# Kernel tuning notes

Hardware: AMD Instinct MI355X
Metric: run time of the kernel (lower is better)

Reference implementation:

```python
import jax, jax.numpy as jnp
import numpy as np

B, S, D = 2, 2048, 1024
H = 16
HD = D // H

def setup_inputs() -> dict:
    key = jax.random.key(0)
    ks = jax.random.split(key, 9)
    scale = 1.0 / np.sqrt(D)
    return {
        "qi": jax.random.normal(ks[0], (B, S, D), jnp.float32),
        "ki": jax.random.normal(ks[1], (B, S, D), jnp.float32),
        "vi": jax.random.normal(ks[2], (B, S, D), jnp.float32),
        "Wq": jax.random.normal(ks[3], (D, D), jnp.float32) * scale,
        "Wq_def": jax.random.normal(ks[4], (D, D), jnp.float32) * scale,
        "Wk": jax.random.normal(ks[5], (D, D), jnp.float32) * scale,
        "Wk_def": jax.random.normal(ks[6], (D, D), jnp.float32) * scale,
        "Wv": jax.random.normal(ks[7], (D, D), jnp.float32) * scale,
        "Wo": jax.random.normal(ks[8], (D, D), jnp.float32) * scale,
    }

def _heads(x, W):
    # torch Linear: x @ W.T, then view (B,S,H,HD) and transpose -> (B,H,S,HD)
    return (x @ W.T).reshape(B, S, H, HD).transpose(0, 2, 1, 3)

def reference(qi, ki, vi, Wq, Wq_def, Wk, Wk_def, Wv, Wo):
    q = _heads(qi, Wq)
    q_def = _heads(qi, Wq_def)
    k = _heads(ki, Wk)
    k_def = _heads(ki, Wk_def)
    v = _heads(vi, Wv)
    inv_sqrt = 1.0 / jnp.sqrt(jnp.asarray(HD, qi.dtype))
    scores = jnp.einsum('bhse,bhte->bhst', q, k) * inv_sqrt
    def_scores = jnp.einsum('bhse,bhte->bhst', q_def, k_def) * inv_sqrt
    # defeasible weights: sigmoid(def_scores).sum over t -> [B,H,S], broadcast over query dim
    def_w = jax.nn.sigmoid(def_scores).sum(axis=3)  # [B,H,S]
    attn = jax.nn.softmax(scores * def_w[:, :, None, :], axis=-1)
    attended = jnp.einsum('bhst,bhtd->bshd', attn, v).reshape(B, S, D)
    return attended @ Wo.T
```

## Files before the change

### kernel.cpp

```cpp
#include <hip/hip_runtime.h>
#include <math.h>

#define BSZ 2
#define SEQ 2048
#define DIM 1024
#define NH 16
#define HDIM 64
#define MR (BSZ*SEQ)

typedef __attribute__((ext_vector_type(8))) short bf16x8;
typedef __attribute__((ext_vector_type(4))) short bf16x4;
typedef __attribute__((ext_vector_type(4))) float floatx4;
typedef _Float16 f16x8 __attribute__((ext_vector_type(8)));

static __device__ __forceinline__ unsigned short f2bf(float x) {
    unsigned u = __float_as_uint(x);
    u += 0x7fffu + ((u >> 16) & 1u);
    return (unsigned short)(u >> 16);
}
static __device__ __forceinline__ float bf2f(unsigned short h) {
    return __uint_as_float(((unsigned)h) << 16);
}
static __device__ __forceinline__ unsigned short f2h(float x) {
    union { _Float16 h; unsigned short u; } v;
    v.h = (_Float16)x;
    return v.u;
}
static __device__ __forceinline__ float fexp2(float x) {
#if __has_builtin(__builtin_amdgcn_exp2f)
    return __builtin_amdgcn_exp2f(x);
#else
    return __expf(x * 0.69314718055994531f);
#endif
}
static __device__ __forceinline__ bf16x4 pack_bf16x4(float a, float b, float c, float d) {
    union { unsigned u[2]; bf16x4 v; } r;
    asm("v_cvt_pk_bf16_f32 %0, %1, %2" : "=v"(r.u[0]) : "v"(a), "v"(b));
    asm("v_cvt_pk_bf16_f32 %0, %1, %2" : "=v"(r.u[1]) : "v"(c), "v"(d));
    return r.v;
}
#define MFMA16(a,b,c) __builtin_amdgcn_mfma_f32_16x16x32_bf16((a),(b),(c),0,0,0)

static __device__ __forceinline__ floatx4 mfma_f16(bf16x8 a, bf16x8 b, floatx4 c) {
    union { bf16x8 s; f16x8 h; } ua, ub;
    ua.s = a; ub.s = b;
    return __builtin_amdgcn_mfma_f32_16x16x32_f16(ua.h, ub.h, c, 0, 0, 0);
}

static __device__ __forceinline__ floatx4 pv_mfma(bf16x4 a, bf16x4 b, floatx4 c) {
#if __has_builtin(__builtin_amdgcn_mfma_f32_16x16x16bf16_1k)
    return __builtin_amdgcn_mfma_f32_16x16x16bf16_1k(a, b, c, 0, 0, 0);
#else
    bf16x8 a8 = {a[0],a[1],a[2],a[3],0,0,0,0};
    bf16x8 b8 = {b[0],b[1],b[2],b[3],0,0,0,0};
    return MFMA16(a8, b8, c);
#endif
}

static __device__ __forceinline__ void gld16(const void* g, void* l) {
    __builtin_amdgcn_global_load_lds(
        (const __attribute__((address_space(1))) void*)g,
        (__attribute__((address_space(3))) void*)l, 16, 0, 0);
}

__global__ __launch_bounds__(256)
void conv_split(const float* p0, const float* p1, const float* p2,
                const float* p3,
                unsigned short* o0, unsigned short* o1, unsigned short* o2,
                unsigned short* o3,
                int r0, int r1, int r2, int r3)
{
    const float* pin; unsigned short* pout; int rows;
    switch (blockIdx.y) {
        case 0: pin=p0; pout=o0; rows=r0; break;
        case 1: pin=p1; pout=o1; rows=r1; break;
        case 2: pin=p2; pout=o2; rows=r2; break;
        default: pin=p3; pout=o3; rows=r3; break;
    }
    size_t idx = (size_t)blockIdx.x * 256 + threadIdx.x;
    if (idx * 4 >= (size_t)rows * DIM) return;
    size_t row = (idx * 4) >> 10;
    int col = (int)((idx * 4) & 1023);
    float4 f = *(const float4*)(pin + idx * 4);
    ushort4 h, l;
    h.x = f2bf(f.x); l.x = f2bf(f.x - bf2f(h.x));
    h.y = f2bf(f.y); l.y = f2bf(f.y - bf2f(h.y));
    h.z = f2bf(f.z); l.z = f2bf(f.z - bf2f(h.z));
    h.w = f2bf(f.w); l.w = f2bf(f.w - bf2f(h.w));
    *(ushort4*)(pout + row * 2048 + col)        = h;
    *(ushort4*)(pout + row * 2048 + 1024 + col) = l;
}

__global__ __launch_bounds__(256)
void conv_f16(const float* p0, const float* p1, const float* p2, const float* p3,
              unsigned short* o0, unsigned short* o1, unsigned short* o2,
              unsigned short* o3, int r0, int r1, int r2, int r3)
{
    const float* pin; unsigned short* pout; int rows;
    switch (blockIdx.y) {
        case 0: pin=p0; pout=o0; rows=r0; break;
        case 1: pin=p1; pout=o1; rows=r1; break;
        case 2: pin=p2; pout=o2; rows=r2; break;
        default: pin=p3; pout=o3; rows=r3; break;
    }
    size_t idx = (size_t)blockIdx.x * 256 + threadIdx.x;
    if (idx * 4 >= (size_t)rows * DIM) return;
    float4 f = *(const float4*)(pin + idx * 4);
    ushort4 h;
    h.x = f2h(f.x); h.y = f2h(f.y); h.z = f2h(f.z); h.w = f2h(f.w);
    *(ushort4*)(pout + idx * 4) = h;
}

__global__ __launch_bounds__(256)
void conv_hi(const float* p0, const float* p1, const float* p2,
             unsigned short* o0, unsigned short* o1, unsigned short* o2,
             int n0, int n1, int n2)
{
    const float* pin; unsigned short* pout; int n;
    switch (blockIdx.y) {
        case 0: pin=p0; pout=o0; n=n0; break;
        case 1: pin=p1; pout=o1; n=n1; break;
        default: pin=p2; pout=o2; n=n2; break;
    }
    size_t idx = (size_t)blockIdx.x * 256 + threadIdx.x;
    if (idx * 4 >= (size_t)n) return;
    float4 f = *(const float4*)(pin + idx * 4);
    ushort4 h;
    h.x = f2bf(f.x); h.y = f2bf(f.y); h.z = f2bf(f.z); h.w = f2bf(f.w);
    *(ushort4*)(pout + idx * 4) = h;
}

template<int EPI, bool SPLIT3, int DT>
__global__ __launch_bounds__(256)
void gemm_mfma(const unsigned short* __restrict__ A0, const unsigned short* __restrict__ A1,
               const unsigned short* __restrict__ B0, const unsigned short* __restrict__ B1,
               void* C0v, void* C1v, int lda, int ldb, int nkb)
{
    const unsigned short* A = blockIdx.z ? A1 : A0;
    const unsigned short* B = blockIdx.z ? B1 : B0;
    float* Cf = (float*)(blockIdx.z ? C1v : C0v);
    unsigned short* Cb = (unsigned short*)(blockIdx.z ? C1v : C0v);

    __shared__ __align__(16) unsigned short As[128][64];
    __shared__ __align__(16) unsigned short Bs[128][64];

    const int tid = threadIdx.x;
    const int lane = tid & 63, wv = tid >> 6;
    const int c = lane & 15, quad = lane >> 4;
    const int wm = wv >> 1, wn = wv & 1;
    const int rowBase = blockIdx.y << 7;
    const int colBase = blockIdx.x << 7;

    floatx4 acc[4][4];
#pragma unroll
    for (int i = 0; i < 4; ++i)
#pragma unroll
        for (int j = 0; j < 4; ++j) acc[i][j] = (floatx4){0.f,0.f,0.f,0.f};

    for (int kb = 0; kb < nkb; ++kb) {
        int aoff, boff;
        if (SPLIT3) {
            int t = kb >> 4, kk = (kb & 15) << 6;
            aoff = ((t == 1) ? 1024 : 0) + kk;
            boff = ((t == 2) ? 1024 : 0) + kk;
        } else { aoff = boff = kb << 6; }
        __syncthreads();
#pragma unroll
        for (int i = 0; i < 4; ++i) {
            int f = tid + (i << 8);
            int r = f >> 3, ch = (f & 7) << 3;
            gld16(A + (size_t)(rowBase + r) * lda + aoff + ch,
                  &As[0][0] + (size_t)f * 8);
            gld16(B + (size_t)(colBase + r) * ldb + boff + ch,
                  &Bs[0][0] + (size_t)f * 8);
        }
        __syncthreads();
#pragma unroll
        for (int ks = 0; ks < 2; ++ks) {
            bf16x8 af[4], bfr[4];
#pragma unroll
            for (int i = 0; i < 4; ++i) {
                af[i]  = *(const bf16x8*)&As[wm*64 + i*16 + c][ks*32 + quad*8];
                bfr[i] = *(const bf16x8*)&Bs[wn*64 + i*16 + c][ks*32 + quad*8];
            }
#pragma unroll
            for (int mi = 0; mi < 4; ++mi)
#pragma unroll
                for (int ni = 0; ni < 4; ++ni) {
                    if (DT == 0) acc[mi][ni] = MFMA16(af[mi], bfr[ni], acc[mi][ni]);
                    else         acc[mi][ni] = mfma_f16(af[mi], bfr[ni], acc[mi][ni]);
                }
        }
    }
    const int row0 = rowBase + wm*64 + quad*4;
    if (EPI == 0) {
        const int col0 = colBase + wn*64 + c;
#pragma unroll
        for (int mi = 0; mi < 4; ++mi)
#pragma unroll
            for (int r = 0; r < 4; ++r) {
                size_t ro = (size_t)(row0 + mi*16 + r) * 1024 + col0;
#pragma unroll
                for (int ni = 0; ni < 4; ++ni)
                    Cf[ro + ni*16] = acc[mi][ni][r];
            }
    } else if (EPI == 1) {
        const int h = (colBase >> 6) + wn;
#pragma unroll
        for (int mi = 0; mi < 4; ++mi)
#pragma unroll
            for (int r = 0; r < 4; ++r) {
                int row = row0 + mi*16 + r;
                int b = row >> 11, s = row & 2047;
                size_t base = ((size_t)((b<<4) | h) * 2048 + s) * 128;
                const int sw = (s & 7) << 3;
#pragma unroll
                for (int ni = 0; ni < 4; ++ni) {
                    int d = ni*16 + c;
                    int dsw = d ^ sw;
                    float x = acc[mi][ni][r];
                    unsigned short hb = f2bf(x);
                    Cb[base + dsw]      = hb;
                    Cb[base + 64 + dsw] = f2bf(x - bf2f(hb));
                }
            }
    } else if (EPI == 2) {
        const int h = (colBase >> 6) + wn;
#pragma unroll
        for (int mi = 0; mi < 4; ++mi) {
            int row = row0 + mi*16;
            int b = row >> 11, s = row & 2047;
#pragma unroll
            for (int ni = 0; ni < 4; ++ni) {
                int d = ni*16 + c;
                int scol = s ^ ((d & 7) << 3);
                size_t base = ((size_t)((b<<4)|h) * 64 + d) * 2048 + scol;
                ushort4 o4;
                o4.x = f2bf(acc[mi][ni][0]); o4.y = f2bf(acc[mi][ni][1]);
                o4.z = f2bf(acc[mi][ni][2]); o4.w = f2bf(acc[mi][ni][3]);
                *(ushort4*)(Cb + base) = o4;
            }
        }
    } else {
        const int h = (colBase >> 6) + wn;
#pragma unroll
        for (int mi = 0; mi < 4; ++mi)
#pragma unroll
            for (int r = 0; r < 4; ++r) {
                int row = row0 + mi*16 + r;
                int b = row >> 11, s = row & 2047;
                size_t base = ((size_t)((b<<4) | h) * 2048 + s) * 64;
#pragma unroll
                for (int ni = 0; ni < 4; ++ni)
                    Cb[base + ni*16 + c] = f2h(acc[mi][ni][r]);
            }
    }
}

__global__ __launch_bounds__(512)
void defw_mfma(const unsigned short* __restrict__ qd,
               const unsigned short* __restrict__ kd,
               float* __restrict__ defw)
{
    __shared__ __align__(16) unsigned short Ks[64][72];
    const int tid = threadIdx.x;
    const int wv = tid >> 6, lane = tid & 63;
    const int c = lane & 15, quad = lane >> 4;
    const int bh = blockIdx.y;
    const int qbase = blockIdx.x << 7;
    const int trow = tid >> 3, seg = tid & 7;

    bf16x8 qf[2];
    {
        const unsigned short* qrow =
            qd + ((size_t)bh*2048 + qbase + wv*16 + c)*64 + quad*8;
        qf[0] = *(const bf16x8*)(qrow);
        qf[1] = *(const bf16x8*)(qrow + 32);
    }
    float rs[4] = {0.f,0.f,0.f,0.f};
    const unsigned short* kbase = kd + (size_t)bh*2048*64;
    bf16x8 kpre = *(const bf16x8*)(kbase + (size_t)trow*64 + seg*8);
    for (int kt = 0; kt < SEQ; kt += 64) {
        __syncthreads();
        *(bf16x8*)&Ks[trow][seg*8] = kpre;
        __syncthreads();
        if (kt + 64 < SEQ)
            kpre = *(const bf16x8*)(kbase + (size_t)(kt + 64 + trow)*64 + seg*8);
#pragma unroll
        for (int nk = 0; nk < 4; ++nk) {
            const unsigned short* kr = &Ks[16*nk + c][quad*8];
            bf16x8 k0 = *(const bf16x8*)(kr);
            bf16x8 k1 = *(const bf16x8*)(kr + 32);
            floatx4 s = {0.f,0.f,0.f,0.f};
            s = mfma_f16(qf[0], k0, s);
            s = mfma_f16(qf[1], k1, s);
#pragma unroll
            for (int r = 0; r < 4; ++r)
                rs[r] += 1.f / (1.f + __expf(-0.125f * s[r]));
        }
    }
#pragma unroll
    for (int r = 0; r < 4; ++r) {
        float vv = rs[r];
        vv += __shfl_xor(vv, 1, 16);
        vv += __shfl_xor(vv, 2, 16);
        vv += __shfl_xor(vv, 4, 16);
        vv += __shfl_xor(vv, 8, 16);
        if (c == 0)
            defw[(size_t)bh*SEQ + qbase + wv*16 + 4*quad + r]
                = vv * 0.18033688011112042f;
    }
}

__global__ __launch_bounds__(512)
void flash_mfma(const unsigned short* __restrict__ q,
                const unsigned short* __restrict__ kk,
                const unsigned short* __restrict__ vt,
                const float* __restrict__ dwg,
                unsigned short* __restrict__ o)
{
    __shared__ __align__(16) unsigned short Ks[2][64][128];
    __shared__ __align__(16) unsigned short Vs[2][64][64];
    __shared__ __align__(16) float dwL[SEQ];
    const int tid = threadIdx.x;
    const int wv = tid >> 6, lane = tid & 63;
    const int c = lane & 15, quad = lane >> 4;
    const int cswz = c & 7;
    const int bh = blockIdx.y, b = bh >> 4, h = bh & 15;
    const int qbase = blockIdx.x << 7;

    const unsigned short* kbase = kk + (size_t)bh*2048*128;
    const unsigned short* vbase = vt + (size_t)bh*64*2048;

    bf16x8 qhi[2], qlo[2];
    {
        const unsigned short* qrow =
            q + ((size_t)bh*2048 + qbase + wv*16 + c)*128;
        qhi[0] = *(const bf16x8*)(qrow + (((quad     ) ^ cswz) << 3));
        qhi[1] = *(const bf16x8*)(qrow + (((quad +  4) ^ cswz) << 3));
        qlo[0] = *(const bf16x8*)(qrow + (((quad +  8) ^ cswz) << 3));
        qlo[1] = *(const bf16x8*)(qrow + (((quad + 12) ^ cswz) << 3));
    }
    gld16(dwg + (size_t)bh*SEQ + (size_t)tid*4, &dwL[(wv*64) * 4]);
#pragma unroll
    for (int i = 0; i < 2; ++i) {
        int flat = tid + (i << 9);
        int r = flat >> 4, ch = flat & 15;
        gld16(kbase + (size_t)r*128 + (ch << 3),
              &Ks[0][0][0] + ((wv*64 + (i << 9)) << 3));
    }
    {
        int d = tid >> 3, ch = tid & 7;
        gld16(vbase + (size_t)d*2048 + (ch << 3),
              &Vs[0][0][0] + (wv*64 << 3));
    }

    floatx4 Oa[4];
#pragma unroll
    for (int nd = 0; nd < 4; ++nd) Oa[nd] = (floatx4){0.f,0.f,0.f,0.f};
    float mrun = -3.0e38f, lrun = 0.f;

#define FLASH_TILE(CUR, KT, PF)                                               \
    {                                                                         \
        __builtin_amdgcn_s_barrier();                                         \
        if (PF) {                                                             \
            _Pragma("unroll")                                                 \
            for (int i = 0; i < 2; ++i) {                                     \
                int flat = tid + (i << 9);                                    \
                int r = flat >> 4, ch = flat & 15;                            \
                gld16(kbase + (size_t)((KT) + 64 + r)*128 + (ch << 3),        \
                      &Ks[(CUR)^1][0][0] + ((wv*64 + (i << 9)) << 3));        \
            }                                                                 \
            {                                                                 \
                int d = tid >> 3, ch = tid & 7;                               \
                gld16(vbase + (size_t)d*2048 + ((KT) + 64) + (ch << 3),       \
                      &Vs[(CUR)^1][0][0] + (wv*64 << 3));                     \
            }                                                                 \
            asm volatile("s_waitcnt vmcnt(3)" ::: "memory");                  \
        } else {                                                              \
            asm volatile("s_waitcnt vmcnt(0)" ::: "memory");                  \
        }                                                                     \
        __builtin_amdgcn_s_barrier();                                         \
        __builtin_amdgcn_sched_barrier(0);                                    \
        float z[4][4];                                                        \
        _Pragma("unroll")                                                     \
        for (int nk = 0; nk < 4; ++nk) {                                      \
            const unsigned short* krow = &Ks[CUR][16*nk + c][0];              \
            bf16x8 kh0 = *(const bf16x8*)(krow + (((quad     ) ^ cswz) << 3));\
            bf16x8 kh1 = *(const bf16x8*)(krow + (((quad +  4) ^ cswz) << 3));\
            bf16x8 kl0 = *(const bf16x8*)(krow + (((quad +  8) ^ cswz) << 3));\
            bf16x8 kl1 = *(const bf16x8*)(krow + (((quad + 12) ^ cswz) << 3));\
            float4 d4 = *(const float4*)&dwL[(KT) + nk*16 + quad*4];          \
            floatx4 s = {0.f,0.f,0.f,0.f};                                    \
            __builtin_amdgcn_s_setprio(1);                                    \
            s = MFMA16(kh0, qhi[0], s);                                       \
            s = MFMA16(kh1, qhi[1], s);                                       \
            s = MFMA16(kh0, qlo[0], s);                                       \
            s = MFMA16(kh1, qlo[1], s);                                       \
            s = MFMA16(kl0, qhi[0], s);                                       \
            s = MFMA16(kl1, qhi[1], s);                                       \
            __builtin_amdgcn_s_setprio(0);                                    \
            z[nk][0] = s[0] * d4.x;                                           \
            z[nk][1] = s[1] * d4.y;                                           \
            z[nk][2] = s[2] * d4.z;                                           \
            z[nk][3] = s[3] * d4.w;                                           \
        }                                                                     \
        {                                                                     \
            float tm = z[0][0];                                               \
            _Pragma("unroll")                                                 \
            for (int nk = 0; nk < 4; ++nk)                                    \
                _Pragma("unroll")                                             \
                for (int r = 0; r < 4; ++r) tm = fmaxf(tm, z[nk][r]);         \
            tm = fmaxf(tm, __shfl_xor(tm, 16));                               \
            tm = fmaxf(tm, __shfl_xor(tm, 32));                               \
            if (__any(tm > mrun)) {                                           \
                float mn = fmaxf(mrun, tm);                                   \
                float al = fexp2(mrun - mn);                                  \
                mrun = mn;                                                    \
                lrun *= al;                                                   \
                _Pragma("unroll")                                             \
                for (int nd = 0; nd < 4; ++nd)                                \
                    _Pragma("unroll")                                         \
                    for (int r = 0; r < 4; ++r)                               \
                        Oa[nd][r] *= al;                                      \
            }                                                                 \
            float rsum = 0.f;                                                 \
            _Pragma("unroll")                                                 \
            for (int nk = 0; nk < 4; ++nk)                                    \
                _Pragma("unroll")                                             \
                for (int r = 0; r < 4; ++r) {                                 \
                    z[nk][r] = fexp2(z[nk][r] - mrun);                        \
                    rsum += z[nk][r];                                         \
                }                                                             \
            rsum += __shfl_xor(rsum, 16);                                     \
            rsum += __shfl_xor(rsum, 32);                                     \
            lrun += rsum;                                                     \
        }                                                                     \
        bf16x4 pb[4];                                                         \
        _Pragma("unroll")                                                     \
        for (int nk = 0; nk < 4; ++nk)                                        \
            pb[nk] = pack_bf16x4(z[nk][0], z[nk][1], z[nk][2], z[nk][3]);     \
        __builtin_amdgcn_s_setprio(1);                                        \
        _Pragma("unroll")                                                     \
        for (int ks = 0; ks < 4; ++ks) {                                      \
            const int vch = ((2*ks + (quad >> 1)) ^ cswz);                    \
            _Pragma("unroll")                                                 \
            for (int nd = 0; nd < 4; ++nd) {                                  \
                const bf16x4 va = *(const bf16x4*)                            \
                    (&Vs[CUR][nd*16 + c][0] + (vch << 3) + ((quad & 1) << 2));\
                Oa[nd] = pv_mfma(va, pb[ks], Oa[nd]);                         \
            }                                                                 \
        }                                                                     \
        __builtin_amdgcn_s_setprio(0);                                        \
    }

    for (int kt = 0; kt < SEQ; kt += 128) {
        FLASH_TILE(0, kt, 1)
        FLASH_TILE(1, kt + 64, kt + 128 < SEQ)
    }
#undef FLASH_TILE

    {
        float invl = 1.f / lrun;
        int s_abs = qbase + wv*16 + c;
        unsigned short* orow = o + ((size_t)(b*SEQ + s_abs))*DIM + h*HDIM;
#pragma unroll
        for (int nd = 0; nd < 4; ++nd) {
            ushort4 o4;
            o4.x = f2bf(Oa[nd][0] * invl);
            o4.y = f2bf(Oa[nd][1] * invl);
            o4.z = f2bf(Oa[nd][2] * invl);
            o4.w = f2bf(Oa[nd][3] * invl);
            *(ushort4*)(orow + nd*16 + quad*4) = o4;
        }
    }
}

extern "C" void kernel_launch(void* const* d_in, const int* in_sizes, int n_in,
                              void* d_out, int out_size, void* d_ws, size_t ws_size,
                              hipStream_t stream)
{
    (void)in_sizes; (void)n_in; (void)out_size; (void)ws_size;
    const float* qi     = (const float*)d_in[0];
    const float* ki     = (const float*)d_in[1];
    const float* vi     = (const float*)d_in[2];
    const float* Wq     = (const float*)d_in[3];
    const float* Wq_def = (const float*)d_in[4];
    const float* Wk     = (const float*)d_in[5];
    const float* Wk_def = (const float*)d_in[6];
    const float* Wv     = (const float*)d_in[7];
    const float* Wo     = (const float*)d_in[8];
    float* out = (float*)d_out;

    char* ws = (char*)d_ws;
    const size_t MB = 1024 * 1024;
    unsigned short* Aqf  = (unsigned short*)(ws +  0*MB);
    unsigned short* Akf  = (unsigned short*)(ws +  8*MB);
    unsigned short* Bqdf = (unsigned short*)(ws + 16*MB);
    unsigned short* Bkdf = (unsigned short*)(ws + 18*MB);
    unsigned short* qdf  = (unsigned short*)(ws + 20*MB);
    unsigned short* kdf  = (unsigned short*)(ws + 28*MB);
    unsigned short* Aq  = (unsigned short*)(ws +  0*MB);
    unsigned short* Ak  = (unsigned short*)(ws + 16*MB);
    unsigned short* Bq  = (unsigned short*)(ws + 32*MB);
    unsigned short* Bk  = (unsigned short*)(ws + 36*MB);
    unsigned short* qs  = (unsigned short*)(ws + 40*MB);
    unsigned short* ks  = (unsigned short*)(ws + 56*MB);
    float*          dw  = (float*)(ws + 72*MB);
    unsigned short* Av  = (unsigned short*)(ws +  0*MB);
    unsigned short* Bv  = (unsigned short*)(ws +  8*MB);
    unsigned short* Bo  = (unsigned short*)(ws + 10*MB);
    unsigned short* Vt  = (unsigned short*)(ws + 12*MB);
    unsigned short* att = (unsigned short*)(ws + 20*MB);

    dim3 cb(256);
    dim3 gP(DIM/128, MR/128, 2);
    dim3 gS(DIM/128, MR/128, 1);
    dim3 gA(SEQ/128, BSZ*NH);

    conv_f16<<<dim3(4096, 4), cb, 0, stream>>>(
        qi, ki, Wq_def, Wk_def, Aqf, Akf, Bqdf, Bkdf, MR, MR, DIM, DIM);
    gemm_mfma<3, false, 1><<<gP, cb, 0, stream>>>(Aqf, Akf, Bqdf, Bkdf, qdf, kdf, 1024, 1024, 16);
    defw_mfma<<<gA, dim3(512), 0, stream>>>(qdf, kdf, dw);
    conv_split<<<dim3(4096, 4), cb, 0, stream>>>(
        qi, ki, Wq, Wk, Aq, Ak, Bq, Bk, MR, MR, DIM, DIM);
    gemm_mfma<1, true, 0><<<gP, cb, 0, stream>>>(Aq, Ak, Bq, Bk, qs, ks, 2048, 2048, 48);
    conv_hi<<<dim3(4096, 3), cb, 0, stream>>>(vi, Wv, Wo, Av, Bv, Bo,
                                              MR*DIM, DIM*DIM, DIM*DIM);
    gemm_mfma<2, false, 0><<<gS, cb, 0, stream>>>(Av, Av, Bv, Bv, Vt, Vt, 1024, 1024, 16);
    flash_mfma<<<gA, dim3(512), 0, stream>>>(qs, ks, Vt, dw, att);
    gemm_mfma<0, false, 0><<<gS, cb, 0, stream>>>(att, att, Bo, Bo, out, out, 1024, 1024, 16);
}
```

Measured before the change: 444.6 us.

## Prefetch next GEMM K-tile into registers and pad LDS rows

Replaces the direct global-to-LDS loads with register prefetching: the next K-block is loaded from global memory into registers while MFMAs run on the current tile, then written to LDS at the top of the next iteration. LDS rows are padded from 64 to 72 elements to reduce bank conflicts on the fragment reads. This costs more VGPRs for the staging registers and more LDS, which could lower occupancy.

After: 416.6 us. -6.3%, faster.

```diff
diff --git a/kernel.cpp b/kernel.cpp
--- a/kernel.cpp
+++ b/kernel.cpp
@@ -141,8 +141,8 @@
     float* Cf = (float*)(blockIdx.z ? C1v : C0v);
     unsigned short* Cb = (unsigned short*)(blockIdx.z ? C1v : C0v);
 
-    __shared__ __align__(16) unsigned short As[128][64];
-    __shared__ __align__(16) unsigned short Bs[128][64];
+    __shared__ __align__(16) unsigned short As[128][72];
+    __shared__ __align__(16) unsigned short Bs[128][72];
 
     const int tid = threadIdx.x;
     const int lane = tid & 63, wv = tid >> 6;
@@ -157,24 +157,41 @@
 #pragma unroll
         for (int j = 0; j < 4; ++j) acc[i][j] = (floatx4){0.f,0.f,0.f,0.f};
 
-    for (int kb = 0; kb < nkb; ++kb) {
-        int aoff, boff;
-        if (SPLIT3) {
-            int t = kb >> 4, kk = (kb & 15) << 6;
-            aoff = ((t == 1) ? 1024 : 0) + kk;
-            boff = ((t == 2) ? 1024 : 0) + kk;
-        } else { aoff = boff = kb << 6; }
-        __syncthreads();
+    bf16x8 ar[4], br[4];
+    {
 #pragma unroll
         for (int i = 0; i < 4; ++i) {
             int f = tid + (i << 8);
-            int r = f >> 3, ch = (f & 7) << 3;
-            gld16(A + (size_t)(rowBase + r) * lda + aoff + ch,
-                  &As[0][0] + (size_t)f * 8);
-            gld16(B + (size_t)(colBase + r) * ldb + boff + ch,
-                  &Bs[0][0] + (size_t)f * 8);
-        }
+            int r = f >> 3, kbk = (f & 7) << 3;
+            ar[i] = *(const bf16x8*)(A + (size_t)(rowBase + r) * lda + kbk);
+            br[i] = *(const bf16x8*)(B + (size_t)(colBase + r) * ldb + kbk);
+        }
+    }
+    for (int kb = 0; kb < nkb; ++kb) {
         __syncthreads();
+#pragma unroll
+        for (int i = 0; i < 4; ++i) {
+            int f = tid + (i << 8);
+            int r = f >> 3, kbk = (f & 7) << 3;
+            *(bf16x8*)&As[r][kbk] = ar[i];
+            *(bf16x8*)&Bs[r][kbk] = br[i];
+        }
+        __syncthreads();
+        if (kb + 1 < nkb) {
+            int kn = kb + 1, aoff, boff;
+            if (SPLIT3) {
+                int t = kn >> 4, kk = (kn & 15) << 6;
+                aoff = ((t == 1) ? 1024 : 0) + kk;
+                boff = ((t == 2) ? 1024 : 0) + kk;
+            } else { aoff = boff = kn << 6; }
+#pragma unroll
+            for (int i = 0; i < 4; ++i) {
+                int f = tid + (i << 8);
+                int r = f >> 3, kbk = (f & 7) << 3;
+                ar[i] = *(const bf16x8*)(A + (size_t)(rowBase + r) * lda + aoff + kbk);
+                br[i] = *(const bf16x8*)(B + (size_t)(colBase + r) * ldb + boff + kbk);
+            }
+        }
 #pragma unroll
         for (int ks = 0; ks < 2; ++ks) {
             bf16x8 af[4], bfr[4];
```

## Double-buffer GEMM shared-memory tiles to overlap global loads with MFMA

Applied to the files above, without the earlier changes.

The MFMA GEMM now uses two shared-memory buffers per operand. While the current K-tile is being computed, the next tile is already loading, with explicit vmcnt waits and raw s_barrier calls in place of the old load-sync-compute loop. This is meant to hide global-to-LDS load latency behind matrix math. It doubles LDS use to 64KB per block, which can lower occupancy. The manually unrolled-by-two loop also assumes nkb is even.

New measurement: 441.0 us. About the same (-0.8%).

```diff
diff --git a/kernel.cpp b/kernel.cpp
--- a/kernel.cpp
+++ b/kernel.cpp
@@ -141,8 +141,8 @@
     float* Cf = (float*)(blockIdx.z ? C1v : C0v);
     unsigned short* Cb = (unsigned short*)(blockIdx.z ? C1v : C0v);
 
-    __shared__ __align__(16) unsigned short As[128][64];
-    __shared__ __align__(16) unsigned short Bs[128][64];
+    __shared__ __align__(16) unsigned short As[2][128][64];
+    __shared__ __align__(16) unsigned short Bs[2][128][64];
 
     const int tid = threadIdx.x;
     const int lane = tid & 63, wv = tid >> 6;
@@ -157,41 +157,62 @@
 #pragma unroll
         for (int j = 0; j < 4; ++j) acc[i][j] = (floatx4){0.f,0.f,0.f,0.f};
 
-    for (int kb = 0; kb < nkb; ++kb) {
-        int aoff, boff;
-        if (SPLIT3) {
-            int t = kb >> 4, kk = (kb & 15) << 6;
-            aoff = ((t == 1) ? 1024 : 0) + kk;
-            boff = ((t == 2) ? 1024 : 0) + kk;
-        } else { aoff = boff = kb << 6; }
-        __syncthreads();
-#pragma unroll
-        for (int i = 0; i < 4; ++i) {
-            int f = tid + (i << 8);
-            int r = f >> 3, ch = (f & 7) << 3;
-            gld16(A + (size_t)(rowBase + r) * lda + aoff + ch,
-                  &As[0][0] + (size_t)f * 8);
-            gld16(B + (size_t)(colBase + r) * ldb + boff + ch,
-                  &Bs[0][0] + (size_t)f * 8);
-        }
-        __syncthreads();
-#pragma unroll
-        for (int ks = 0; ks < 2; ++ks) {
-            bf16x8 af[4], bfr[4];
-#pragma unroll
-            for (int i = 0; i < 4; ++i) {
-                af[i]  = *(const bf16x8*)&As[wm*64 + i*16 + c][ks*32 + quad*8];
-                bfr[i] = *(const bf16x8*)&Bs[wn*64 + i*16 + c][ks*32 + quad*8];
-            }
-#pragma unroll
-            for (int mi = 0; mi < 4; ++mi)
-#pragma unroll
-                for (int ni = 0; ni < 4; ++ni) {
-                    if (DT == 0) acc[mi][ni] = MFMA16(af[mi], bfr[ni], acc[mi][ni]);
-                    else         acc[mi][ni] = mfma_f16(af[mi], bfr[ni], acc[mi][ni]);
-                }
-        }
-    }
+#define GSTAGE(BUF, KN)                                                       \
+    {                                                                         \
+        int aoff, boff;                                                       \
+        if (SPLIT3) {                                                         \
+            int t = (KN) >> 4, kk = ((KN) & 15) << 6;                         \
+            aoff = ((t == 1) ? 1024 : 0) + kk;                                \
+            boff = ((t == 2) ? 1024 : 0) + kk;                                \
+        } else { aoff = boff = (KN) << 6; }                                   \
+        _Pragma("unroll")                                                     \
+        for (int i = 0; i < 4; ++i) {                                         \
+            int f = tid + (i << 8);                                           \
+            int r = f >> 3, ch = (f & 7) << 3;                                \
+            gld16(A + (size_t)(rowBase + r) * lda + aoff + ch,                \
+                  &As[BUF][0][0] + (size_t)f * 8);                            \
+            gld16(B + (size_t)(colBase + r) * ldb + boff + ch,                \
+                  &Bs[BUF][0][0] + (size_t)f * 8);                            \
+        }                                                                     \
+    }
+
+#define GEMM_TILE(CUR, KB)                                                    \
+    {                                                                         \
+        __builtin_amdgcn_s_barrier();                                         \
+        if ((KB) + 1 < nkb) {                                                 \
+            GSTAGE((CUR)^1, (KB)+1);                                          \
+            asm volatile("s_waitcnt vmcnt(8)" ::: "memory");                  \
+        } else {                                                              \
+            asm volatile("s_waitcnt vmcnt(0)" ::: "memory");                  \
+        }                                                                     \
+        __builtin_amdgcn_s_barrier();                                         \
+        __builtin_amdgcn_sched_barrier(0);                                    \
+        _Pragma("unroll")                                                     \
+        for (int ks = 0; ks < 2; ++ks) {                                      \
+            bf16x8 af[4], bfr[4];                                             \
+            _Pragma("unroll")                                                 \
+            for (int i = 0; i < 4; ++i) {                                     \
+                af[i]  = *(const bf16x8*)&As[CUR][wm*64 + i*16 + c][ks*32 + quad*8]; \
+                bfr[i] = *(const bf16x8*)&Bs[CUR][wn*64 + i*16 + c][ks*32 + quad*8]; \
+            }                                                                 \
+            _Pragma("unroll")                                                 \
+            for (int mi = 0; mi < 4; ++mi)                                    \
+                _Pragma("unroll")                                             \
+                for (int ni = 0; ni < 4; ++ni) {                              \
+                    if (DT == 0) acc[mi][ni] = MFMA16(af[mi], bfr[ni], acc[mi][ni]); \
+                    else         acc[mi][ni] = mfma_f16(af[mi], bfr[ni], acc[mi][ni]); \
+                }                                                             \
+        }                                                                     \
+    }
+
+    GSTAGE(0, 0)
+    for (int kb = 0; kb < nkb; kb += 2) {
+        GEMM_TILE(0, kb)
+        GEMM_TILE(1, kb + 1)
+    }
+#undef GEMM_TILE
+#undef GSTAGE
+
     const int row0 = rowBase + wm*64 + quad*4;
     if (EPI == 0) {
         const int col0 = colBase + wn*64 + c;
```
